# Kernel optimization log

Hardware: AMD Instinct MI355X
Metric: run time of the kernel (lower is better)

## Reference

```python
import jax, jax.numpy as jnp
import numpy as np
import math

P = 256   # state_dim
H = 1024  # hidden_dim
B = 8     # batch
L = 4096  # sequence length
R_MIN, R_MAX, THETA_MAX = 0.9, 0.999, math.pi


def _map_theta_to_A(thetas, G_diag, steps):
    cos_t = jnp.cos(thetas)
    tan_sq = jnp.tan(thetas) ** 2
    sqrt_term = 4.0 * jnp.sqrt(steps ** 4 / cos_t ** 2 + steps ** 5 * G_diag / cos_t ** 2)
    common = steps ** 2 * (-4.0 - 2.0 * steps * G_diag - 4.0 * tan_sq - 2.0 * steps * G_diag * tan_sq)
    denom = 2.0 * steps ** 4 * (1.0 + tan_sq)
    A_plus = (sqrt_term - common) / denom
    A_minus = (-sqrt_term - common) / denom
    return jnp.where(thetas > math.pi / 2, A_plus, A_minus)


def setup_inputs() -> dict:
    key = jax.random.key(0)
    k1, k2, k3, k4, k5, k6, k7 = jax.random.split(key, 7)
    x = jax.random.normal(k1, (B, L, H), dtype=jnp.float32)
    steps_raw = 0.5 * jax.random.normal(k2, (P,), dtype=jnp.float32)
    steps = jax.nn.sigmoid(steps_raw)
    mags = jnp.sqrt(jax.random.uniform(k3, (P,)) * (R_MAX ** 2 - R_MIN ** 2) + R_MIN ** 2)
    G_raw = (1.0 - mags ** 2) / (steps * mags ** 2)
    theta = jax.random.uniform(k4, (P,)) * THETA_MAX
    A_raw = _map_theta_to_A(theta, jax.nn.relu(G_raw), steps)
    std_b = 1.0 / math.sqrt(H)
    B_mat = jax.random.uniform(k5, (P, H, 2), minval=-std_b, maxval=std_b, dtype=jnp.float32)
    std_c = 1.0 / math.sqrt(P)
    C_mat = jax.random.uniform(k6, (H, P, 2), minval=-std_c, maxval=std_c, dtype=jnp.float32)
    D_vec = jax.random.normal(k7, (H,), dtype=jnp.float32)
    return {"input_sequence": x, "steps_raw": steps_raw, "G_raw": G_raw,
            "A_raw": A_raw, "B_mat": B_mat, "C_mat": C_mat, "D_vec": D_vec}


def _binary_operator(q_i, q_j):
    """Compose (M, F) pairs: (Mj@Mi, Mj@Fi + Fj); M flattened as [M11,M12,M21,M22] (4P)."""
    A_i, b_i = q_i
    A_j, b_j = q_j
    iA, iB, iC, iD = jnp.split(A_i, 4, axis=-1)
    jA, jB, jC, jD = jnp.split(A_j, 4, axis=-1)
    A_new = jnp.concatenate([jA * iA + jB * iC, jA * iB + jB * iD,
                             jC * iA + jD * iC, jC * iB + jD * iD], axis=-1)
    b_i1, b_i2 = jnp.split(b_i, 2, axis=-2)  # (..., P, 2) each
    new_b1 = jA[..., None] * b_i1 + jB[..., None] * b_i2
    new_b2 = jC[..., None] * b_i1 + jD[..., None] * b_i2
    return A_new, jnp.concatenate([new_b1, new_b2], axis=-2) + b_j


def _forward(x, steps_raw, G_raw, A_raw, B_mat, C_mat, D_vec):
    steps = jax.nn.sigmoid(steps_raw)          # (P,)
    G_diag = jax.nn.relu(G_raw)
    A_diag = jax.nn.relu(A_raw)

    Bu = jnp.einsum('blh,pht->blpt', x, B_mat)  # (B, L, P, 2)

    S = 1.0 + steps * G_diag                    # (P,)
    alpha = steps ** 2 * A_diag / S
    alpha = 1.99 * jnp.tanh(alpha / 1.99)
    M = jnp.concatenate([1.0 / S, -alpha / steps, steps / S, 1.0 - alpha])  # (4P,)
    M_exp = jnp.broadcast_to(M, (x.shape[0], x.shape[1], 4 * steps.shape[0]))

    step_b = steps[None, None, :, None]
    S_b = S[None, None, :, None]
    F1 = step_b * (1.0 / S_b) * Bu
    F2 = step_b ** 2 * (1.0 / S_b) * Bu
    F_mat = jnp.concatenate([F1, F2], axis=-2)  # (B, L, 2P, 2)

    _, xs = jax.lax.associative_scan(_binary_operator, (M_exp, F_mat), axis=1)
    ys = xs[..., steps.shape[0]:, :]            # (B, L, P, 2) -- the x-states

    Cy = jnp.einsum('blpt,hpt->blht', ys, C_mat)  # (B, L, H, 2)
    return Cy[..., 0] - Cy[..., 1] + x * D_vec


def reference(input_sequence, steps_raw, G_raw, A_raw, B_mat, C_mat, D_vec):
    return _forward(input_sequence, steps_raw, G_raw, A_raw, B_mat, C_mat, D_vec)
```

## Files before the change

kernel.cpp:

```cpp
#include <hip/hip_runtime.h>
#include <math.h>
#include <stdint.h>

#define PCH 256
#define HD  1024
#define BB  8
#define LL  4096
#define NN  512
#define MROWS (BB*LL)
#define NCH 64
#define TCH 64

typedef __bf16 bf16x8 __attribute__((ext_vector_type(8)));
typedef float  f32x4  __attribute__((ext_vector_type(4)));
typedef short  s16x8  __attribute__((ext_vector_type(8)));

#define OFFB_W1    ((size_t)0)
#define OFFB_C2    (OFFB_W1  + (size_t)NN*HD*2)
#define OFFB_CST   (OFFB_C2  + (size_t)HD*NN*2)
#define OFFB_BU    (OFFB_CST + (size_t)16384)
#define OFFB_YS    (OFFB_BU  + (size_t)MROWS*NN*2)
#define OFFB_ZEND  (OFFB_YS  + (size_t)MROWS*NN*2)
#define OFFB_CARRY (OFFB_ZEND + (size_t)BB*NCH*2*NN*4)

__device__ __forceinline__ short f2bf(float f) {
    union { float f; uint32_t u; } v; v.f = f;
    uint32_t r = v.u + 0x7FFFu + ((v.u >> 16) & 1u);
    return (short)(r >> 16);
}
__device__ __forceinline__ float bf2f(unsigned short u) {
    union { uint32_t u; float f; } v; v.u = ((uint32_t)u) << 16;
    return v.f;
}

__global__ void prep_consts(const float* __restrict__ steps_raw,
                            const float* __restrict__ G_raw,
                            const float* __restrict__ A_raw,
                            float* __restrict__ cst) {
    int p = threadIdx.x;
    if (p >= PCH) return;
    float steps = 1.0f / (1.0f + expf(-steps_raw[p]));
    float G = fmaxf(G_raw[p], 0.0f);
    float A = fmaxf(A_raw[p], 0.0f);
    float S = 1.0f + steps * G;
    float alpha = steps * steps * A / S;
    alpha = 1.99f * tanhf(alpha / 1.99f);
    float m11 = 1.0f / S;
    float m12 = -alpha / steps;
    float m21 = steps / S;
    float m22 = 1.0f - alpha;
    float c1 = steps / S;
    float c2 = steps * steps / S;
    float a = 1.f, b = 0.f, c = 0.f, d = 1.f;
    for (int i = 0; i < TCH; ++i) {
        float na = m11*a + m12*c;
        float nb = m11*b + m12*d;
        float nc = m21*a + m22*c;
        float nd = m21*b + m22*d;
        a = na; b = nb; c = nc; d = nd;
    }
    cst[0*PCH+p] = m11; cst[1*PCH+p] = m12; cst[2*PCH+p] = m21; cst[3*PCH+p] = m22;
    cst[4*PCH+p] = c1;  cst[5*PCH+p] = c2;
    cst[6*PCH+p] = a;   cst[7*PCH+p] = b;   cst[8*PCH+p] = c;   cst[9*PCH+p] = d;
}

__global__ void prep_w(const float* __restrict__ B_mat,
                       const float* __restrict__ C_mat,
                       short* __restrict__ W1t,
                       short* __restrict__ C2t) {
    int idx = blockIdx.x * blockDim.x + threadIdx.x;
    if (idx >= HD * NN) return;
    {
        int n = idx >> 10;
        int h = idx & (HD - 1);
        int p = n >> 1, t = n & 1;
        W1t[idx] = f2bf(B_mat[(size_t)p * HD * 2 + (size_t)h * 2 + t]);
    }
    {
        int h = idx >> 9;
        int n = idx & (NN - 1);
        int p = n >> 1, t = n & 1;
        float sgn = (t == 0) ? 1.0f : -1.0f;
        C2t[idx] = f2bf(sgn * C_mat[(size_t)h * PCH * 2 + (size_t)p * 2 + t]);
    }
}

template <int K, int N>
__global__ __launch_bounds__(256, 3)
void gemm128_cvtA(const float* __restrict__ Af32, const short* __restrict__ Bt,
                  unsigned short* __restrict__ Cout) {
    __shared__ alignas(16) char smem[32768];
    constexpr int GX = N / 128;
    const int nwg = gridDim.x;
    const int cpx = nwg >> 3;
    const int bid = blockIdx.x;
    const int wg = (bid & 7) * cpx + (bid >> 3);
    const int by = wg / GX, bx = wg % GX;
    const int m0 = by * 128, n0 = bx * 128;

    const int tid = threadIdx.x;
    const int lane = tid & 63, w = tid >> 6;
    const int wm = w >> 1, wn = w & 1;
    const int g = lane >> 4, r16 = lane & 15;

    auto stageB = [&](int buf, int k0) {
        #pragma unroll
        for (int s = 0; s < 2; ++s) {
            int c = tid + s * 256;
            int row = c >> 2, q = c & 3;
            int gq = q ^ ((row >> 1) & 3);
            const short* sb = Bt + (size_t)(n0 + row) * K + k0 + gq * 8;
            __builtin_amdgcn_global_load_lds(
                (const __attribute__((address_space(1))) void*)sb,
                (__attribute__((address_space(3))) void*)(smem + buf * 16384 + 8192 + c * 16),
                16, 0, 0);
        }
    };
    f32x4 av0, av1, av2, av3;
    auto loadAf32 = [&](int k0) {
        {
            int c = tid;
            int row = c >> 2, q = c & 3;
            const f32x4* px = (const f32x4*)(Af32 + (size_t)(m0 + row) * K + k0 + q * 8);
            av0 = px[0]; av1 = px[1];
        }
        {
            int c = tid + 256;
            int row = c >> 2, q = c & 3;
            const f32x4* px = (const f32x4*)(Af32 + (size_t)(m0 + row) * K + k0 + q * 8);
            av2 = px[0]; av3 = px[1];
        }
    };
    auto writeAf32 = [&](int buf) {
        {
            int c = tid;
            int row = c >> 2, q = c & 3;
            int gq = q ^ ((row >> 1) & 3);
            s16x8 r;
            #pragma unroll
            for (int j = 0; j < 4; ++j) { r[j] = f2bf(av0[j]); r[4 + j] = f2bf(av1[j]); }
            *(s16x8*)(smem + buf * 16384 + row * 64 + gq * 16) = r;
        }
        {
            int c = tid + 256;
            int row = c >> 2, q = c & 3;
            int gq = q ^ ((row >> 1) & 3);
            s16x8 r;
            #pragma unroll
            for (int j = 0; j < 4; ++j) { r[j] = f2bf(av2[j]); r[4 + j] = f2bf(av3[j]); }
            *(s16x8*)(smem + buf * 16384 + row * 64 + gq * 16) = r;
        }
    };

    const int swzg = (g ^ ((r16 >> 1) & 3)) << 4;
    int aoff[4], boff[4];
    #pragma unroll
    for (int i = 0; i < 4; ++i)
        aoff[i] = (wm * 64 + i * 16 + r16) * 64 + swzg;
    #pragma unroll
    for (int j = 0; j < 4; ++j)
        boff[j] = 8192 + (wn * 64 + j * 16 + r16) * 64 + swzg;

    f32x4 acc[4][4];
    #pragma unroll
    for (int i = 0; i < 4; ++i)
        #pragma unroll
        for (int j = 0; j < 4; ++j) acc[i][j] = (f32x4)0.0f;

    constexpr int NT = K / 32;
    loadAf32(0); stageB(0, 0); writeAf32(0);
    __syncthreads();
    int cur = 0;
    #pragma unroll 1
    for (int t = 0; t < NT; ++t) {
        if (t + 1 < NT) {
            loadAf32((t + 1) * 32);
            stageB(cur ^ 1, (t + 1) * 32);
        }
        const char* base = smem + cur * 16384;
        bf16x8 af[4], bfv[4];
        #pragma unroll
        for (int i = 0; i < 4; ++i) af[i] = *(const bf16x8*)(base + aoff[i]);
        #pragma unroll
        for (int j = 0; j < 4; ++j) bfv[j] = *(const bf16x8*)(base + boff[j]);
        #pragma unroll
        for (int i = 0; i < 4; ++i)
            #pragma unroll
            for (int j = 0; j < 4; ++j)
                acc[i][j] = __builtin_amdgcn_mfma_f32_16x16x32_bf16(
                    af[i], bfv[j], acc[i][j], 0, 0, 0);
        if (t + 1 < NT) writeAf32(cur ^ 1);
        __syncthreads();
        cur ^= 1;
    }

    const int crow0 = m0 + wm * 64 + g * 4;
    const int ccol0 = n0 + wn * 64 + r16;
    #pragma unroll
    for (int j = 0; j < 4; ++j) {
        int col = ccol0 + j * 16;
        #pragma unroll
        for (int i = 0; i < 4; ++i) {
            #pragma unroll
            for (int r = 0; r < 4; ++r) {
                size_t idx = (size_t)(crow0 + i * 16 + r) * N + col;
                Cout[idx] = (unsigned short)f2bf(acc[i][j][r]);
            }
        }
    }
}

template <int K, int N, bool EPI>
__global__ __launch_bounds__(512, 2)
void gemm256(const short* __restrict__ A, const short* __restrict__ Bt,
             float* __restrict__ Cout, const float* __restrict__ xres,
             const float* __restrict__ Dv) {
    __shared__ alignas(16) char smem[131072];
    constexpr int GX = N / 256;
    const int nwg = gridDim.x;
    const int cpx = nwg >> 3;
    const int bid = blockIdx.x;
    const int wg = (bid & 7) * cpx + (bid >> 3);
    const int by = wg / GX, bx = wg % GX;
    const int m0 = by * 256, n0 = bx * 256;

    const int tid = threadIdx.x;
    const int lane = tid & 63, w = tid >> 6;
    const int wm = w >> 2, wn = w & 3;
    const int g = lane >> 4, r16 = lane & 15;

    auto stage = [&](int buf, int k0) {
        #pragma unroll
        for (int s = 0; s < 4; ++s) {
            int c = tid + s * 512;
            int row = c >> 3, q = c & 7;
            int gq = q ^ (row & 7);
            const short* sa = A + (size_t)(m0 + row) * K + k0 + gq * 8;
            __builtin_amdgcn_global_load_lds(
                (const __attribute__((address_space(1))) void*)sa,
                (__attribute__((address_space(3))) void*)(smem + buf * 65536 + c * 16),
                16, 0, 0);
        }
        #pragma unroll
        for (int s = 0; s < 4; ++s) {
            int c = tid + s * 512;
            int row = c >> 3, q = c & 7;
            int gq = q ^ (row & 7);
            const short* sb = Bt + (size_t)(n0 + row) * K + k0 + gq * 8;
            __builtin_amdgcn_global_load_lds(
                (const __attribute__((address_space(1))) void*)sb,
                (__attribute__((address_space(3))) void*)(smem + buf * 65536 + 32768 + c * 16),
                16, 0, 0);
        }
    };

    int aoff[8], boff[4];
    #pragma unroll
    for (int mi = 0; mi < 8; ++mi) {
        int ra = wm * 128 + mi * 16 + r16;
        aoff[mi] = ra * 128 + ((g ^ (ra & 7)) << 4);
    }
    #pragma unroll
    for (int nj = 0; nj < 4; ++nj) {
        int rb = wn * 64 + nj * 16 + r16;
        boff[nj] = 32768 + rb * 128 + ((g ^ (rb & 7)) << 4);
    }

    f32x4 acc[8][4];
    #pragma unroll
    for (int mi = 0; mi < 8; ++mi)
        #pragma unroll
        for (int nj = 0; nj < 4; ++nj) acc[mi][nj] = (f32x4)0.0f;

    constexpr int NT = K / 64;
    stage(0, 0);
    __syncthreads();
    int cur = 0;
    #pragma unroll 1
    for (int t = 0; t < NT; ++t) {
        if (t + 1 < NT) stage(cur ^ 1, (t + 1) * 64);
        const char* base = smem + cur * 65536;
        #pragma unroll
        for (int kk = 0; kk < 2; ++kk) {
            bf16x8 af[8], bfv[4];
            #pragma unroll
            for (int mi = 0; mi < 8; ++mi)
                af[mi] = *(const bf16x8*)(base + (aoff[mi] ^ (kk << 6)));
            #pragma unroll
            for (int nj = 0; nj < 4; ++nj)
                bfv[nj] = *(const bf16x8*)(base + (boff[nj] ^ (kk << 6)));
            #pragma unroll
            for (int mi = 0; mi < 8; ++mi)
                #pragma unroll
                for (int nj = 0; nj < 4; ++nj)
                    acc[mi][nj] = __builtin_amdgcn_mfma_f32_16x16x32_bf16(
                        af[mi], bfv[nj], acc[mi][nj], 0, 0, 0);
        }
        __syncthreads();
        cur ^= 1;
    }

    const int crow0 = m0 + wm * 128 + g * 4;
    const int ccol0 = n0 + wn * 64 + r16;
    #pragma unroll
    for (int nj = 0; nj < 4; ++nj) {
        int col = ccol0 + nj * 16;
        float dv = EPI ? Dv[col] : 0.0f;
        #pragma unroll
        for (int mi = 0; mi < 8; ++mi) {
            #pragma unroll
            for (int r = 0; r < 4; ++r) {
                size_t idx = (size_t)(crow0 + mi * 16 + r) * N + col;
                float v = acc[mi][nj][r];
                if (EPI) v = fmaf(xres[idx], dv, v);
                Cout[idx] = v;
            }
        }
    }
}

__global__ __launch_bounds__(512)
void scan_phase1(const unsigned short* __restrict__ Bu, const float* __restrict__ cst,
                 float* __restrict__ zend) {
    int bid = blockIdx.x;
    int b = bid / NCH, c = bid % NCH;
    int n = threadIdx.x;
    int p = n >> 1;
    float m11 = cst[0*PCH+p], m12 = cst[1*PCH+p], m21 = cst[2*PCH+p], m22 = cst[3*PCH+p];
    float c1 = cst[4*PCH+p], c2 = cst[5*PCH+p];
    float s1 = 0.f, s2 = 0.f;
    const unsigned short* bp = Bu + ((size_t)(b * LL + c * TCH)) * NN + n;
    #pragma unroll 4
    for (int i = 0; i < TCH; ++i) {
        float u = bf2f(bp[(size_t)i * NN]);
        float ns1 = fmaf(m11, s1, fmaf(m12, s2, c1 * u));
        float ns2 = fmaf(m21, s1, fmaf(m22, s2, c2 * u));
        s1 = ns1; s2 = ns2;
    }
    size_t base = ((size_t)(b * NCH + c) * 2) * NN + n;
    zend[base] = s1;
    zend[base + NN] = s2;
}

__global__ __launch_bounds__(512)
void scan_phase2(const float* __restrict__ zend, const float* __restrict__ cst,
                 float* __restrict__ carry) {
    int b = blockIdx.x;
    int n = threadIdx.x;
    int p = n >> 1;
    float a = cst[6*PCH+p], bm = cst[7*PCH+p], cmt = cst[8*PCH+p], d = cst[9*PCH+p];
    float cs1 = 0.f, cs2 = 0.f;
    for (int c = 0; c < NCH; ++c) {
        size_t base = ((size_t)(b * NCH + c) * 2) * NN + n;
        float z1 = zend[base], z2 = zend[base + NN];
        float ns1 = fmaf(a, cs1, fmaf(bm, cs2, z1));
        float ns2 = fmaf(cmt, cs1, fmaf(d, cs2, z2));
        carry[base] = ns1;
        carry[base + NN] = ns2;
        cs1 = ns1; cs2 = ns2;
    }
}

__global__ __launch_bounds__(512)
void scan_phase3(const unsigned short* __restrict__ Bu, const float* __restrict__ cst,
                 const float* __restrict__ carry, unsigned short* __restrict__ ys) {
    int bid = blockIdx.x;
    int b = bid / NCH, c = bid % NCH;
    int n = threadIdx.x;
    int p = n >> 1;
    float m11 = cst[0*PCH+p], m12 = cst[1*PCH+p], m21 = cst[2*PCH+p], m22 = cst[3*PCH+p];
    float c1 = cst[4*PCH+p], c2 = cst[5*PCH+p];
    float s1 = 0.f, s2 = 0.f;
    if (c > 0) {
        size_t base = ((size_t)(b * NCH + (c - 1)) * 2) * NN + n;
        s1 = carry[base];
        s2 = carry[base + NN];
    }
    const unsigned short* bp = Bu + ((size_t)(b * LL + c * TCH)) * NN + n;
    unsigned short* yp = ys + ((size_t)(b * LL + c * TCH)) * NN + n;
    #pragma unroll 4
    for (int i = 0; i < TCH; ++i) {
        float u = bf2f(bp[(size_t)i * NN]);
        float ns1 = fmaf(m11, s1, fmaf(m12, s2, c1 * u));
        float ns2 = fmaf(m21, s1, fmaf(m22, s2, c2 * u));
        s1 = ns1; s2 = ns2;
        yp[(size_t)i * NN] = (unsigned short)f2bf(s2);
    }
}

extern "C" void kernel_launch(void* const* d_in, const int* in_sizes, int n_in,
                              void* d_out, int out_size, void* d_ws, size_t ws_size,
                              hipStream_t stream) {
    const float* x         = (const float*)d_in[0];
    const float* steps_raw = (const float*)d_in[1];
    const float* G_raw     = (const float*)d_in[2];
    const float* A_raw     = (const float*)d_in[3];
    const float* B_mat     = (const float*)d_in[4];
    const float* C_mat     = (const float*)d_in[5];
    const float* D_vec     = (const float*)d_in[6];
    float* out = (float*)d_out;
    char*  ws  = (char*)d_ws;

    short*          W1t   = (short*)(ws + OFFB_W1);
    short*          C2t   = (short*)(ws + OFFB_C2);
    float*          cst   = (float*)(ws + OFFB_CST);
    unsigned short* Bu    = (unsigned short*)(ws + OFFB_BU);
    unsigned short* ysbf  = (unsigned short*)(ws + OFFB_YS);
    float*          zend  = (float*)(ws + OFFB_ZEND);
    float*          carry = (float*)(ws + OFFB_CARRY);

    prep_consts<<<1, 256, 0, stream>>>(steps_raw, G_raw, A_raw, cst);
    prep_w<<<(HD * NN) / 512, 512, 0, stream>>>(B_mat, C_mat, W1t, C2t);

    gemm128_cvtA<HD, NN><<<(NN / 128) * (MROWS / 128), 256, 0, stream>>>(
        x, W1t, Bu);

    scan_phase1<<<BB * NCH, 512, 0, stream>>>(Bu, cst, zend);
    scan_phase2<<<BB, 512, 0, stream>>>(zend, cst, carry);
    scan_phase3<<<BB * NCH, 512, 0, stream>>>(Bu, cst, carry, ysbf);

    gemm256<NN, HD, true><<<(HD / 256) * (MROWS / 256), 512, 0, stream>>>(
        (const short*)ysbf, C2t, out, x, D_vec);
}
```

Baseline: 199.1 us.

## Enlarge first GEMM tile to 256x256 with BK=64 and 8 waves

The input-projection GEMM (fp32 x converted to bf16 on the fly) moves from 128x128 tiles with 4 waves and K-step 32 to 256x256 tiles with 8 waves, K-step 64 and 128 KB of shared memory. Each wave now computes a 128x64 sub-tile, with a new 8-way XOR swizzle for the 128-byte LDS rows. The larger tile is meant to cut redundant global reads of x and the weights and raise MFMA work per barrier. In exchange it uses more registers and LDS per block, and the grid shrinks to 256 blocks, which may leave CUs underfilled.

New measurement: 180.6 us. 1.1x faster.

```diff
diff --git a/kernel.cpp b/kernel.cpp
--- a/kernel.cpp
+++ b/kernel.cpp
@@ -86,125 +86,120 @@
 }
 
 template <int K, int N>
-__global__ __launch_bounds__(256, 3)
-void gemm128_cvtA(const float* __restrict__ Af32, const short* __restrict__ Bt,
+__global__ __launch_bounds__(512, 2)
+void gemm256_cvtA(const float* __restrict__ Af32, const short* __restrict__ Bt,
                   unsigned short* __restrict__ Cout) {
-    __shared__ alignas(16) char smem[32768];
-    constexpr int GX = N / 128;
+    __shared__ alignas(16) char smem[131072];
+    constexpr int GX = N / 256;
     const int nwg = gridDim.x;
     const int cpx = nwg >> 3;
     const int bid = blockIdx.x;
     const int wg = (bid & 7) * cpx + (bid >> 3);
     const int by = wg / GX, bx = wg % GX;
-    const int m0 = by * 128, n0 = bx * 128;
+    const int m0 = by * 256, n0 = bx * 256;
 
     const int tid = threadIdx.x;
     const int lane = tid & 63, w = tid >> 6;
-    const int wm = w >> 1, wn = w & 1;
+    const int wm = w >> 2, wn = w & 3;
     const int g = lane >> 4, r16 = lane & 15;
 
     auto stageB = [&](int buf, int k0) {
         #pragma unroll
-        for (int s = 0; s < 2; ++s) {
-            int c = tid + s * 256;
-            int row = c >> 2, q = c & 3;
-            int gq = q ^ ((row >> 1) & 3);
+        for (int s = 0; s < 4; ++s) {
+            int c = tid + s * 512;
+            int row = c >> 3, q = c & 7;
+            int gq = q ^ (row & 7);
             const short* sb = Bt + (size_t)(n0 + row) * K + k0 + gq * 8;
             __builtin_amdgcn_global_load_lds(
                 (const __attribute__((address_space(1))) void*)sb,
-                (__attribute__((address_space(3))) void*)(smem + buf * 16384 + 8192 + c * 16),
+                (__attribute__((address_space(3))) void*)(smem + buf * 65536 + 32768 + c * 16),
                 16, 0, 0);
         }
     };
-    f32x4 av0, av1, av2, av3;
-    auto loadAf32 = [&](int k0) {
-        {
-            int c = tid;
-            int row = c >> 2, q = c & 3;
-            const f32x4* px = (const f32x4*)(Af32 + (size_t)(m0 + row) * K + k0 + q * 8);
-            av0 = px[0]; av1 = px[1];
-        }
-        {
-            int c = tid + 256;
-            int row = c >> 2, q = c & 3;
-            const f32x4* px = (const f32x4*)(Af32 + (size_t)(m0 + row) * K + k0 + q * 8);
-            av2 = px[0]; av3 = px[1];
+    f32x4 av[4][2];
+    auto loadA = [&](int k0) {
+        #pragma unroll
+        for (int s = 0; s < 4; ++s) {
+            int c = tid + s * 512;
+            int row = c >> 3, q = c & 7;
+            int gq = q ^ (row & 7);
+            const f32x4* px = (const f32x4*)(Af32 + (size_t)(m0 + row) * K + k0 + gq * 8);
+            av[s][0] = px[0]; av[s][1] = px[1];
         }
     };
-    auto writeAf32 = [&](int buf) {
-        {
-            int c = tid;
-            int row = c >> 2, q = c & 3;
-            int gq = q ^ ((row >> 1) & 3);
+    auto writeA = [&](int buf) {
+        #pragma unroll
+        for (int s = 0; s < 4; ++s) {
+            int c = tid + s * 512;
+            int row = c >> 3, q = c & 7;
             s16x8 r;
             #pragma unroll
-            for (int j = 0; j < 4; ++j) { r[j] = f2bf(av0[j]); r[4 + j] = f2bf(av1[j]); }
-            *(s16x8*)(smem + buf * 16384 + row * 64 + gq * 16) = r;
-        }
-        {
-            int c = tid + 256;
-            int row = c >> 2, q = c & 3;
-            int gq = q ^ ((row >> 1) & 3);
-            s16x8 r;
-            #pragma unroll
-            for (int j = 0; j < 4; ++j) { r[j] = f2bf(av2[j]); r[4 + j] = f2bf(av3[j]); }
-            *(s16x8*)(smem + buf * 16384 + row * 64 + gq * 16) = r;
+            for (int j = 0; j < 4; ++j) { r[j] = f2bf(av[s][0][j]); r[4 + j] = f2bf(av[s][1][j]); }
+            *(s16x8*)(smem + buf * 65536 + row * 128 + q * 16) = r;
         }
     };
 
-    const int swzg = (g ^ ((r16 >> 1) & 3)) << 4;
-    int aoff[4], boff[4];
-    #pragma unroll
-    for (int i = 0; i < 4; ++i)
-        aoff[i] = (wm * 64 + i * 16 + r16) * 64 + swzg;
-    #pragma unroll
-    for (int j = 0; j < 4; ++j)
-        boff[j] = 8192 + (wn * 64 + j * 16 + r16) * 64 + swzg;
-
-    f32x4 acc[4][4];
-    #pragma unroll
-    for (int i = 0; i < 4; ++i)
-        #pragma unroll
-        for (int j = 0; j < 4; ++j) acc[i][j] = (f32x4)0.0f;
-
-    constexpr int NT = K / 32;
-    loadAf32(0); stageB(0, 0); writeAf32(0);
+    int aoff[8], boff[4];
+    #pragma unroll
+    for (int mi = 0; mi < 8; ++mi) {
+        int ra = wm * 128 + mi * 16 + r16;
+        aoff[mi] = ra * 128 + ((g ^ (ra & 7)) << 4);
+    }
+    #pragma unroll
+    for (int nj = 0; nj < 4; ++nj) {
+        int rb = wn * 64 + nj * 16 + r16;
+        boff[nj] = 32768 + rb * 128 + ((g ^ (rb & 7)) << 4);
+    }
+
+    f32x4 acc[8][4];
+    #pragma unroll
+    for (int mi = 0; mi < 8; ++mi)
+        #pragma unroll
+        for (int nj = 0; nj < 4; ++nj) acc[mi][nj] = (f32x4)0.0f;
+
+    constexpr int NT = K / 64;
+    loadA(0); stageB(0, 0); writeA(0);
     __syncthreads();
     int cur = 0;
     #pragma unroll 1
     for (int t = 0; t < NT; ++t) {
         if (t + 1 < NT) {
-            loadAf32((t + 1) * 32);
-            stageB(cur ^ 1, (t + 1) * 32);
-        }
-        const char* base = smem + cur * 16384;
-        bf16x8 af[4], bfv[4];
-        #pragma unroll
-        for (int i = 0; i < 4; ++i) af[i] = *(const bf16x8*)(base + aoff[i]);
-        #pragma unroll
-        for (int j = 0; j < 4; ++j) bfv[j] = *(const bf16x8*)(base + boff[j]);
-        #pragma unroll
-        for (int i = 0; i < 4; ++i)
-            #pragma unroll
-            for (int j = 0; j < 4; ++j)
-                acc[i][j] = __builtin_amdgcn_mfma_f32_16x16x32_bf16(
-                    af[i], bfv[j], acc[i][j], 0, 0, 0);
-        if (t + 1 < NT) writeAf32(cur ^ 1);
+            loadA((t + 1) * 64);
+            stageB(cur ^ 1, (t + 1) * 64);
+        }
+        const char* base = smem + cur * 65536;
+        #pragma unroll
+        for (int kk = 0; kk < 2; ++kk) {
+            bf16x8 af[8], bfv[4];
+            #pragma unroll
+            for (int mi = 0; mi < 8; ++mi)
+                af[mi] = *(const bf16x8*)(base + (aoff[mi] ^ (kk << 6)));
+            #pragma unroll
+            for (int nj = 0; nj < 4; ++nj)
+                bfv[nj] = *(const bf16x8*)(base + (boff[nj] ^ (kk << 6)));
+            #pragma unroll
+            for (int mi = 0; mi < 8; ++mi)
+                #pragma unroll
+                for (int nj = 0; nj < 4; ++nj)
+                    acc[mi][nj] = __builtin_amdgcn_mfma_f32_16x16x32_bf16(
+                        af[mi], bfv[nj], acc[mi][nj], 0, 0, 0);
+        }
+        if (t + 1 < NT) writeA(cur ^ 1);
         __syncthreads();
         cur ^= 1;
     }
 
-    const int crow0 = m0 + wm * 64 + g * 4;
+    const int crow0 = m0 + wm * 128 + g * 4;
     const int ccol0 = n0 + wn * 64 + r16;
     #pragma unroll
-    for (int j = 0; j < 4; ++j) {
-        int col = ccol0 + j * 16;
-        #pragma unroll
-        for (int i = 0; i < 4; ++i) {
+    for (int nj = 0; nj < 4; ++nj) {
+        int col = ccol0 + nj * 16;
+        #pragma unroll
+        for (int mi = 0; mi < 8; ++mi) {
             #pragma unroll
             for (int r = 0; r < 4; ++r) {
-                size_t idx = (size_t)(crow0 + i * 16 + r) * N + col;
-                Cout[idx] = (unsigned short)f2bf(acc[i][j][r]);
+                size_t idx = (size_t)(crow0 + mi * 16 + r) * N + col;
+                Cout[idx] = (unsigned short)f2bf(acc[mi][nj][r]);
             }
         }
     }
@@ -412,7 +407,7 @@
     prep_consts<<<1, 256, 0, stream>>>(steps_raw, G_raw, A_raw, cst);
     prep_w<<<(HD * NN) / 512, 512, 0, stream>>>(B_mat, C_mat, W1t, C2t);
 
-    gemm128_cvtA<HD, NN><<<(NN / 128) * (MROWS / 128), 256, 0, stream>>>(
+    gemm256_cvtA<HD, NN><<<(NN / 256) * (MROWS / 256), 512, 0, stream>>>(
         x, W1t, Bu);
 
     scan_phase1<<<BB * NCH, 512, 0, stream>>>(Bu, cst, zend);
```
